# Optimization experiments

Measured on AMD Instinct MI355X. Metric: run time of the kernel, lower is better.

Reference implementation:

```python
import jax, jax.numpy as jnp
import numpy as np

D_MODEL = 1024
N_HEADS = 16
HEAD_DIM = D_MODEL // N_HEADS
B, L = 2, 2048


def setup_inputs() -> dict:
    key = jax.random.key(0)
    ks = jax.random.split(key, 9)
    s = 1.0 / np.sqrt(D_MODEL)
    return {
        "hidden_states": jax.random.normal(ks[0], (B, L, D_MODEL), dtype=jnp.float32),
        "Wq": jax.random.uniform(ks[1], (D_MODEL, D_MODEL), jnp.float32, -s, s),
        "bq": jax.random.uniform(ks[2], (D_MODEL,), jnp.float32, -s, s),
        "Wk": jax.random.uniform(ks[3], (D_MODEL, D_MODEL), jnp.float32, -s, s),
        "bk": jax.random.uniform(ks[4], (D_MODEL,), jnp.float32, -s, s),
        "Wv": jax.random.uniform(ks[5], (D_MODEL, D_MODEL), jnp.float32, -s, s),
        "bv": jax.random.uniform(ks[6], (D_MODEL,), jnp.float32, -s, s),
        "Wo": jax.random.uniform(ks[7], (D_MODEL, D_MODEL), jnp.float32, -s, s),
        "bo": jax.random.uniform(ks[8], (D_MODEL,), jnp.float32, -s, s),
    }


def reference(hidden_states, Wq, bq, Wk, bk, Wv, bv, Wo, bo):
    b, l, d = hidden_states.shape
    h, hd = N_HEADS, HEAD_DIM
    scale = jnp.sqrt(jnp.asarray(hd, hidden_states.dtype))
    # projections (weights stored as [in, out], equivalent to torch Linear W.T)
    Q = (hidden_states @ Wq + bq).reshape(b, l, h, hd).transpose(0, 2, 1, 3)
    K = (hidden_states @ Wk + bk).reshape(b, l, h, hd).transpose(0, 2, 1, 3)
    V = (hidden_states @ Wv + bv).reshape(b, l, h, hd).transpose(0, 2, 1, 3)
    # [b, h, l, l] scores with causal mask
    scores = jnp.einsum("bhqd,bhkd->bhqk", Q, K) / scale
    causal = jnp.tril(jnp.ones((l, l), dtype=bool))
    scores = jnp.where(causal, scores, jnp.asarray(-jnp.inf, scores.dtype))
    weights = jax.nn.softmax(scores, axis=-1)
    out = jnp.einsum("bhqk,bhkd->bhqd", weights, V)
    out = out.transpose(0, 2, 1, 3).reshape(b, l, d)
    return out @ Wo + bo
```

## Files before the change

kernel.cpp:

```cpp
#include <hip/hip_runtime.h>

typedef unsigned short u16;
typedef unsigned int u32;
typedef __attribute__((ext_vector_type(8))) short bf16x8;
typedef __attribute__((ext_vector_type(4))) float f32x4;

__device__ __forceinline__ u16 f2bf(float f) {
    union { float f; u32 u; } x; x.f = f;
    u32 r = x.u + 0x7FFFu + ((x.u >> 16) & 1u);
    return (u16)(r >> 16);
}

__device__ __forceinline__ u16 f2bf_fast(float f) {
    union { float f; u32 u; } x; x.f = f;
    return (u16)((x.u + 0x8000u) >> 16);
}

__device__ __forceinline__ void gload16(const u16* g, u16* l) {
    __builtin_amdgcn_global_load_lds(
        (const __attribute__((address_space(1))) void*)g,
        (__attribute__((address_space(3))) void*)l,
        16, 0, 0);
}

__device__ __forceinline__ f32x4 mfma16(bf16x8 a, bf16x8 b, f32x4 c) {
    return __builtin_amdgcn_mfma_f32_16x16x32_bf16(a, b, c, 0, 0, 0);
}


__global__ __launch_bounds__(256) void cvt_x(const float* __restrict__ in, u16* __restrict__ out, int n4) {
    int i = blockIdx.x * blockDim.x + threadIdx.x;
    if (i >= n4) return;
    float4 v = ((const float4*)in)[i];
    u16* o = out + (size_t)i * 4;
    o[0] = f2bf(v.x); o[1] = f2bf(v.y); o[2] = f2bf(v.z); o[3] = f2bf(v.w);
}

__global__ __launch_bounds__(256) void transpose_w4(const float* __restrict__ Wq, const float* __restrict__ Wk,
                                                    const float* __restrict__ Wv, const float* __restrict__ Wo,
                                                    u16* __restrict__ qkvt, u16* __restrict__ wot) {
    __shared__ float tile[32][33];
    const float* in;
    u16* out;
    if (blockIdx.z == 0)      { in = Wq; out = qkvt; }
    else if (blockIdx.z == 1) { in = Wk; out = qkvt + 1024 * 1024; }
    else if (blockIdx.z == 2) { in = Wv; out = qkvt + 2 * 1024 * 1024; }
    else                      { in = Wo; out = wot; }
    const int bx = blockIdx.x * 32, by = blockIdx.y * 32;
    const int tx = threadIdx.x & 31, ty4 = (threadIdx.x >> 5) * 4;
#pragma unroll
    for (int j = 0; j < 4; ++j)
        tile[ty4 + j][tx] = in[(size_t)(by + ty4 + j) * 1024 + bx + tx];
    __syncthreads();
#pragma unroll
    for (int j = 0; j < 4; ++j)
        out[(size_t)(bx + ty4 + j) * 1024 + by + tx] = f2bf(tile[tx][ty4 + j]);
}

__global__ __launch_bounds__(256) void pack_bias(const float* __restrict__ bq, const float* __restrict__ bk,
                                                 const float* __restrict__ bv, float* __restrict__ out) {
    int i = blockIdx.x * blockDim.x + threadIdx.x;
    if (i >= 3072) return;
    out[i] = (i < 1024) ? bq[i] : ((i < 2048) ? bk[i - 1024] : bv[i - 2048]);
}

template<int MODE>
__global__ __launch_bounds__(256) void gemm128(const u16* __restrict__ A, const u16* __restrict__ Bt,
                                               const float* __restrict__ bias,
                                               u16* __restrict__ oq, u16* __restrict__ ok, u16* __restrict__ ov,
                                               float* __restrict__ of, int K)
{
    __shared__ u16 As[128 * 32];
    __shared__ u16 Bs[128 * 32];

    const int n0 = blockIdx.x * 128;
    const int m0 = blockIdx.y * 128;
    const int t = threadIdx.x;
    const int w = t >> 6, lane = t & 63;
    const int g = lane >> 4, lr = lane & 15;
    const int wm = w >> 1, wn = w & 1;
    const int srow = lane >> 2;
    const int scol = (lane & 3) * 8;

    f32x4 acc[4][4] = {};

    for (int k0 = 0; k0 < K; k0 += 32) {
        __syncthreads();
#pragma unroll
        for (int i = 0; i < 2; ++i) {
            const int c = w + i * 4;
            const int mrow = c * 16 + srow;
            gload16(A  + (size_t)(m0 + mrow) * K + k0 + scol, &As[c * 512 + lane * 8]);
            gload16(Bt + (size_t)(n0 + mrow) * K + k0 + scol, &Bs[c * 512 + lane * 8]);
        }
        __syncthreads();
        bf16x8 af[4], bfr[4];
#pragma unroll
        for (int mi = 0; mi < 4; ++mi) af[mi]  = *(const bf16x8*)&As[(wm * 64 + mi * 16 + lr) * 32 + g * 8];
#pragma unroll
        for (int ni = 0; ni < 4; ++ni) bfr[ni] = *(const bf16x8*)&Bs[(wn * 64 + ni * 16 + lr) * 32 + g * 8];
#pragma unroll
        for (int mi = 0; mi < 4; ++mi)
#pragma unroll
            for (int ni = 0; ni < 4; ++ni)
                acc[mi][ni] = mfma16(af[mi], bfr[ni], acc[mi][ni]);
    }

#pragma unroll
    for (int mi = 0; mi < 4; ++mi) {
#pragma unroll
        for (int ni = 0; ni < 4; ++ni) {
            const int col = n0 + wn * 64 + ni * 16 + lr;
            const int row0 = m0 + wm * 64 + mi * 16 + g * 4;
            const float bs = bias[col];
            if (MODE == 0) {
                const int mat = col >> 10;
                const int nn = col & 1023;
                const int h = nn >> 6, d = nn & 63;
#pragma unroll
                for (int j = 0; j < 4; ++j) {
                    const int rr = row0 + j;
                    const int b = rr >> 11, ll = rr & 2047;
                    const int bh = b * 16 + h;
                    const float v = acc[mi][ni][j] + bs;
                    if (mat == 0)      oq[((size_t)bh * 2048 + ll) * 64 + d] = f2bf(v * 0.1803368801111244f);
                    else if (mat == 1) ok[((size_t)bh * 2048 + ll) * 64 + d] = f2bf(v);
                    else               ov[((size_t)bh * 64 + d) * 2048 + ll] = f2bf(v);
                }
            } else {
#pragma unroll
                for (int j = 0; j < 4; ++j) {
                    const int rr = row0 + j;
                    of[(size_t)rr * 1024 + col] = acc[mi][ni][j] + bs;
                }
            }
        }
    }
}

__global__ __launch_bounds__(256) void attn(const u16* __restrict__ Q, const u16* __restrict__ Kg,
                                            const u16* __restrict__ Vt, u16* __restrict__ O,
                                            float* __restrict__ Opart, float* __restrict__ Mp,
                                            float* __restrict__ Lp, int do_split)
{
    __shared__ u16 Ks[2][64 * 64];
    __shared__ u16 Vs[2][64 * 64];
    __shared__ u16 Ps[4][16 * 64];

    const int bh = blockIdx.x;
    int qb, k_lo, k_hi, split;
    if (!do_split) {
        qb = 31 - (int)blockIdx.y; k_lo = 0; k_hi = qb + 1; split = -1;
    } else {
        const int y = (int)blockIdx.y;
        if (y < 32) {
            qb = 16 + (y >> 1);
            split = y & 1;
            const int mid = (qb + 1) >> 1;
            k_lo = split ? mid : 0;
            k_hi = split ? qb + 1 : mid;
        } else {
            qb = 47 - y; k_lo = 0; k_hi = qb + 1; split = -1;
        }
    }
    const int q0 = qb * 64;
    const int t = threadIdx.x;
    const int w = t >> 6, lane = t & 63;
    const int g = lane >> 4, lr = lane & 15;
    const int qw = q0 + w * 16;
    const int sw = lr & 7;

    const u16* Qb = Q  + (size_t)bh * 2048 * 64;
    const u16* Kb = Kg + (size_t)bh * 2048 * 64;
    const u16* Vb = Vt + (size_t)bh * 64 * 2048;

    const bf16x8 qf0 = *(const bf16x8*)&Qb[(size_t)(qw + lr) * 64 + g * 8];
    const bf16x8 qf1 = *(const bf16x8*)&Qb[(size_t)(qw + lr) * 64 + 32 + g * 8];

    const short one = (short)0x3F80;
    const bf16x8 vones = {one, one, one, one, one, one, one, one};

    f32x4 oacc[4] = {};
    f32x4 lsacc = {};
    float mrun = -1e30f;

    int bpaddr[4];
#pragma unroll
    for (int j = 0; j < 4; ++j) bpaddr[j] = (20 * g + j) * 4;

    const int pw_base = lr * 64;
    const int g2h = g >> 1;
    const int wic2 = (2 * g) & 3;

    bf16x8 kreg[2], vreg[2];
    const int srow0 = t >> 3, sch = t & 7;
    auto issue = [&](int kb) {
#pragma unroll
        for (int i = 0; i < 2; ++i) {
            const int row = srow0 + i * 32;
            kreg[i] = *(const bf16x8*)&Kb[(size_t)(kb * 64 + row) * 64 + sch * 8];
            vreg[i] = *(const bf16x8*)&Vb[(size_t)row * 2048 + kb * 64 + sch * 8];
        }
    };
    auto commit = [&](int buf) {
#pragma unroll
        for (int i = 0; i < 2; ++i) {
            const int row = srow0 + i * 32;
            const int chs = sch ^ (row & 7);
            *(bf16x8*)&Ks[buf][row * 64 + chs * 8] = kreg[i];
            *(bf16x8*)&Vs[buf][row * 64 + chs * 8] = vreg[i];
        }
    };

    issue(k_lo);
    commit(0);

    for (int kb = k_lo; kb < k_hi; ++kb) {
        const int cur = (kb - k_lo) & 1;
        const int k0 = kb * 64;
        __syncthreads();
        const bool more = (kb + 1 < k_hi);
        if (more) issue(kb + 1);

        f32x4 s[4] = {};
        __builtin_amdgcn_s_setprio(1);
#pragma unroll
        for (int ni = 0; ni < 4; ++ni) {
            const int row = ni * 16 + lr;
            bf16x8 kf0 = *(const bf16x8*)&Ks[cur][row * 64 + (g ^ sw) * 8];
            bf16x8 kf1 = *(const bf16x8*)&Ks[cur][row * 64 + ((4 + g) ^ sw) * 8];
            s[ni] = mfma16(kf0, qf0, s[ni]);
            s[ni] = mfma16(kf1, qf1, s[ni]);
        }
        __builtin_amdgcn_s_setprio(0);

        if (kb == qb) {
            const int qq = qw + lr;
#pragma unroll
            for (int ni = 0; ni < 4; ++ni)
#pragma unroll
                for (int j = 0; j < 4; ++j)
                    if (k0 + ni * 16 + g * 4 + j > qq) s[ni][j] = -1e30f;
        }

        float pm = fmaxf(fmaxf(fmaxf(s[0][0], s[0][1]), fmaxf(s[0][2], s[0][3])),
                         fmaxf(fmaxf(s[1][0], s[1][1]), fmaxf(s[1][2], s[1][3])));
        pm = fmaxf(pm, fmaxf(fmaxf(fmaxf(s[2][0], s[2][1]), fmaxf(s[2][2], s[2][3])),
                             fmaxf(fmaxf(s[3][0], s[3][1]), fmaxf(s[3][2], s[3][3]))));
        pm = fmaxf(pm, __shfl_xor(pm, 16));
        pm = fmaxf(pm, __shfl_xor(pm, 32));

        if (__any(pm > mrun + 8.f)) {
            const float mn = fmaxf(mrun, pm);
            const float r = __builtin_amdgcn_exp2f(mrun - mn);
            mrun = mn;
            const int ri = __float_as_int(r);
#pragma unroll
            for (int j = 0; j < 4; ++j) {
                const float ro = __int_as_float(__builtin_amdgcn_ds_bpermute(bpaddr[j], ri));
                lsacc[j] *= ro;
#pragma unroll
                for (int df = 0; df < 4; ++df) oacc[df][j] *= ro;
            }
        }

#pragma unroll
        for (int ni = 0; ni < 4; ++ni) {
            const int c8 = 2 * ni + g2h;
#pragma unroll
            for (int jp = 0; jp < 2; ++jp) {
                const float plo = __builtin_amdgcn_exp2f(s[ni][2 * jp]     - mrun);
                const float phi = __builtin_amdgcn_exp2f(s[ni][2 * jp + 1] - mrun);
                const u32 pr = (u32)f2bf_fast(plo) | ((u32)f2bf_fast(phi) << 16);
                const int wic = wic2 + jp;
                *(u32*)&Ps[w][pw_base + (c8 ^ sw) * 8 + wic * 2] = pr;
            }
        }

        if (more) commit(cur ^ 1);

        const bf16x8 p0 = *(const bf16x8*)&Ps[w][lr * 64 + (g ^ sw) * 8];
        const bf16x8 p1 = *(const bf16x8*)&Ps[w][lr * 64 + ((4 + g) ^ sw) * 8];
        __builtin_amdgcn_s_setprio(1);
        lsacc = mfma16(p0, vones, lsacc);
        lsacc = mfma16(p1, vones, lsacc);
#pragma unroll
        for (int df = 0; df < 4; ++df) {
            const int row = df * 16 + lr;
            bf16x8 vf0 = *(const bf16x8*)&Vs[cur][row * 64 + (g ^ sw) * 8];
            bf16x8 vf1 = *(const bf16x8*)&Vs[cur][row * 64 + ((4 + g) ^ sw) * 8];
            oacc[df] = mfma16(p0, vf0, oacc[df]);
            oacc[df] = mfma16(p1, vf1, oacc[df]);
        }
        __builtin_amdgcn_s_setprio(0);
    }

    if (split < 0) {
        const int b = bh >> 4, h = bh & 15;
#pragma unroll
        for (int j = 0; j < 4; ++j) {
            const float inv = 1.f / lsacc[j];
            const int l = qw + g * 4 + j;
#pragma unroll
            for (int df = 0; df < 4; ++df)
                O[((size_t)b * 2048 + l) * 1024 + h * 64 + df * 16 + lr] = f2bf(oacc[df][j] * inv);
        }
    } else {
        float* Ob = Opart + ((size_t)split * 32 + bh) * (1024 * 64);
        const int rb = qw - 1024 + 4 * g;
#pragma unroll
        for (int j = 0; j < 4; ++j)
#pragma unroll
            for (int df = 0; df < 4; ++df)
                Ob[(size_t)(rb + j) * 64 + df * 16 + lr] = oacc[df][j];
        if (lr == 0) {
#pragma unroll
            for (int j = 0; j < 4; ++j)
                Lp[(split * 32 + bh) * 1024 + rb + j] = lsacc[j];
        }
        if (g == 0)
            Mp[(split * 32 + bh) * 1024 + (qw - 1024) + lr] = mrun;
    }
}

__global__ __launch_bounds__(256) void attn_merge(const float* __restrict__ Opart,
                                                  const float* __restrict__ Mp,
                                                  const float* __restrict__ Lp,
                                                  u16* __restrict__ O)
{
    const int idx = blockIdx.x * 256 + threadIdx.x;
    const int d  = idx & 63;
    const int rr = (idx >> 6) & 1023;
    const int bh = idx >> 16;
    const int si = bh * 1024 + rr;
    const float m0 = Mp[si], m1 = Mp[32 * 1024 + si];
    const float l0 = Lp[si], l1 = Lp[32 * 1024 + si];
    const float M  = fmaxf(m0, m1);
    const float w0 = __builtin_amdgcn_exp2f(m0 - M);
    const float w1 = __builtin_amdgcn_exp2f(m1 - M);
    const float o0 = Opart[(size_t)si * 64 + d];
    const float o1 = Opart[(size_t)(32 * 1024 + si) * 64 + d];
    const float o  = (w0 * o0 + w1 * o1) / (w0 * l0 + w1 * l1);
    const int b = bh >> 4, h = bh & 15;
    const int r = 1024 + rr;
    O[((size_t)b * 2048 + r) * 1024 + h * 64 + d] = f2bf(o);
}


extern "C" void kernel_launch(void* const* d_in, const int* in_sizes, int n_in,
                              void* d_out, int out_size, void* d_ws, size_t ws_size,
                              hipStream_t stream)
{
    const float* hs = (const float*)d_in[0];
    const float* Wq = (const float*)d_in[1];
    const float* bq = (const float*)d_in[2];
    const float* Wk = (const float*)d_in[3];
    const float* bk = (const float*)d_in[4];
    const float* Wv = (const float*)d_in[5];
    const float* bv = (const float*)d_in[6];
    const float* Wo = (const float*)d_in[7];
    const float* bo = (const float*)d_in[8];
    float* out = (float*)d_out;

    char* ws = (char*)d_ws;
    u16*   Xbf   = (u16*)(ws);
    u16*   Wqkvt = (u16*)(ws + (8ull  << 20));
    u16*   Wot   = (u16*)(ws + (14ull << 20));
    float* bqkv  = (float*)(ws + (16ull << 20));
    u16*   Qbuf  = (u16*)(ws + (17ull << 20));
    u16*   Kbuf  = (u16*)(ws + (25ull << 20));
    u16*   Vtbuf = (u16*)(ws + (33ull << 20));
    u16*   Abuf  = Xbf;
    float* Opart = (float*)(ws + (42ull << 20));
    float* Mpart = (float*)(ws + (58ull << 20));
    float* Lpart = (float*)(ws + (58ull << 20) + (512ull << 10));

    const int do_split = (ws_size >= (59ull << 20)) ? 1 : 0;

    cvt_x<<<4096, 256, 0, stream>>>(hs, Xbf, 4096 * 1024 / 4);
    transpose_w4<<<dim3(32, 32, 4), 256, 0, stream>>>(Wq, Wk, Wv, Wo, Wqkvt, Wot);
    pack_bias<<<12, 256, 0, stream>>>(bq, bk, bv, bqkv);

    gemm128<0><<<dim3(24, 32), 256, 0, stream>>>(Xbf, Wqkvt, bqkv, Qbuf, Kbuf, Vtbuf, nullptr, 1024);

    if (do_split) {
        attn<<<dim3(32, 48), 256, 0, stream>>>(Qbuf, Kbuf, Vtbuf, Abuf, Opart, Mpart, Lpart, 1);
        attn_merge<<<8192, 256, 0, stream>>>(Opart, Mpart, Lpart, Abuf);
    } else {
        attn<<<dim3(32, 32), 256, 0, stream>>>(Qbuf, Kbuf, Vtbuf, Abuf, nullptr, nullptr, nullptr, 0);
    }

    gemm128<1><<<dim3(8, 32), 256, 0, stream>>>(Abuf, Wot, bo, nullptr, nullptr, nullptr, out, 1024);
}
```

Before: 135.8 us.

## Deepen GEMM K-tile to 64 with XOR-swizzled LDS and vectorized V stores

The projection GEMM now loads 64-wide K slices per iteration instead of 32, which halves the number of barrier pairs per output tile. LDS rows are XOR-swizzled by chunk to avoid bank conflicts on the 128-byte rows. The transposed V epilogue packs four consecutive bf16 values into one 8-byte store instead of four scalar stores. The cost is doubled LDS use per block, which can reduce occupancy.

```diff
diff --git a/kernel.cpp b/kernel.cpp
--- a/kernel.cpp
+++ b/kernel.cpp
@@ -70,8 +70,8 @@
                                                u16* __restrict__ oq, u16* __restrict__ ok, u16* __restrict__ ov,
                                                float* __restrict__ of, int K)
 {
-    __shared__ u16 As[128 * 32];
-    __shared__ u16 Bs[128 * 32];
+    __shared__ u16 As[128 * 64];
+    __shared__ u16 Bs[128 * 64];
 
     const int n0 = blockIdx.x * 128;
     const int m0 = blockIdx.y * 128;
@@ -79,31 +79,42 @@
     const int w = t >> 6, lane = t & 63;
     const int g = lane >> 4, lr = lane & 15;
     const int wm = w >> 1, wn = w & 1;
-    const int srow = lane >> 2;
-    const int scol = (lane & 3) * 8;
+    const int sw = lr & 7;
+
+    const int srow = lane >> 3;
+    const int schunk = (lane & 7) ^ srow;
+    const u16* pA = A  + (size_t)(m0 + w * 8 + srow) * K + schunk * 8;
+    const u16* pB = Bt + (size_t)(n0 + w * 8 + srow) * K + schunk * 8;
+    u16* lA = &As[w * 512 + lane * 8];
+    u16* lB = &Bs[w * 512 + lane * 8];
+
+    const int sa_row = (wm * 64 + lr) * 64;
+    const int sb_row = (wn * 64 + lr) * 64;
 
     f32x4 acc[4][4] = {};
 
-    for (int k0 = 0; k0 < K; k0 += 32) {
+    for (int k0 = 0; k0 < K; k0 += 64) {
         __syncthreads();
 #pragma unroll
-        for (int i = 0; i < 2; ++i) {
-            const int c = w + i * 4;
-            const int mrow = c * 16 + srow;
-            gload16(A  + (size_t)(m0 + mrow) * K + k0 + scol, &As[c * 512 + lane * 8]);
-            gload16(Bt + (size_t)(n0 + mrow) * K + k0 + scol, &Bs[c * 512 + lane * 8]);
+        for (int i = 0; i < 4; ++i) {
+            gload16(pA + (size_t)i * 32 * K + k0, lA + i * 2048);
+            gload16(pB + (size_t)i * 32 * K + k0, lB + i * 2048);
         }
         __syncthreads();
-        bf16x8 af[4], bfr[4];
-#pragma unroll
-        for (int mi = 0; mi < 4; ++mi) af[mi]  = *(const bf16x8*)&As[(wm * 64 + mi * 16 + lr) * 32 + g * 8];
-#pragma unroll
-        for (int ni = 0; ni < 4; ++ni) bfr[ni] = *(const bf16x8*)&Bs[(wn * 64 + ni * 16 + lr) * 32 + g * 8];
-#pragma unroll
-        for (int mi = 0; mi < 4; ++mi)
-#pragma unroll
-            for (int ni = 0; ni < 4; ++ni)
-                acc[mi][ni] = mfma16(af[mi], bfr[ni], acc[mi][ni]);
+#pragma unroll
+        for (int kk = 0; kk < 2; ++kk) {
+            const int cofs = ((kk * 4 + g) ^ sw) * 8;
+            bf16x8 af[4], bf[4];
+#pragma unroll
+            for (int mi = 0; mi < 4; ++mi) af[mi] = *(const bf16x8*)&As[sa_row + mi * 16 * 64 + cofs];
+#pragma unroll
+            for (int ni = 0; ni < 4; ++ni) bf[ni] = *(const bf16x8*)&Bs[sb_row + ni * 16 * 64 + cofs];
+#pragma unroll
+            for (int mi = 0; mi < 4; ++mi)
+#pragma unroll
+                for (int ni = 0; ni < 4; ++ni)
+                    acc[mi][ni] = mfma16(af[mi], bf[ni], acc[mi][ni]);
+        }
     }
 
 #pragma unroll
@@ -117,22 +128,27 @@
                 const int mat = col >> 10;
                 const int nn = col & 1023;
                 const int h = nn >> 6, d = nn & 63;
-#pragma unroll
-                for (int j = 0; j < 4; ++j) {
-                    const int rr = row0 + j;
-                    const int b = rr >> 11, ll = rr & 2047;
-                    const int bh = b * 16 + h;
-                    const float v = acc[mi][ni][j] + bs;
-                    if (mat == 0)      oq[((size_t)bh * 2048 + ll) * 64 + d] = f2bf(v * 0.1803368801111244f);
-                    else if (mat == 1) ok[((size_t)bh * 2048 + ll) * 64 + d] = f2bf(v);
-                    else               ov[((size_t)bh * 64 + d) * 2048 + ll] = f2bf(v);
+                const int b = row0 >> 11, ll0 = row0 & 2047;
+                const int bh = b * 16 + h;
+                if (mat == 0) {
+#pragma unroll
+                    for (int j = 0; j < 4; ++j)
+                        oq[((size_t)bh * 2048 + ll0 + j) * 64 + d] =
+                            f2bf((acc[mi][ni][j] + bs) * 0.1803368801111244f);
+                } else if (mat == 1) {
+#pragma unroll
+                    for (int j = 0; j < 4; ++j)
+                        ok[((size_t)bh * 2048 + ll0 + j) * 64 + d] = f2bf(acc[mi][ni][j] + bs);
+                } else {
+                    union { ushort4 s4; u16 u[4]; } pk;
+#pragma unroll
+                    for (int j = 0; j < 4; ++j) pk.u[j] = f2bf(acc[mi][ni][j] + bs);
+                    *(ushort4*)&ov[((size_t)bh * 64 + d) * 2048 + ll0] = pk.s4;
                 }
             } else {
 #pragma unroll
-                for (int j = 0; j < 4; ++j) {
-                    const int rr = row0 + j;
-                    of[(size_t)rr * 1024 + col] = acc[mi][ni][j] + bs;
-                }
+                for (int j = 0; j < 4; ++j)
+                    of[(size_t)(row0 + j) * 1024 + col] = acc[mi][ni][j] + bs;
             }
         }
     }
@@ -277,7 +293,7 @@
             }
         }
 
-        if (more) commit(cur ^ 1);
+        if (more) commit((cur ^ 1));
 
         const bf16x8 p0 = *(const bf16x8*)&Ps[w][lr * 64 + (g ^ sw) * 8];
         const bf16x8 p1 = *(const bf16x8*)&Ps[w][lr * 64 + ((4 + g) ^ sw) * 8];
```

Measured after the change: 125.3 us. 7.7% less time.
